# Kernel optimization log

Measured on AMD Instinct MI355X. Metric: run time of the kernel, lower is better.

## Reference

```python
import jax, jax.numpy as jnp
import numpy as np

BOARD = 361  # 19x19 Go board
SEQ = 24     # 8 history boards + 16 move boards


def setup_inputs() -> dict:
    key = jax.random.key(0)
    ks = jax.random.split(key, 12)
    B, H, L = 4096, 256, 2
    s = 1.0 / np.sqrt(H)  # PyTorch LSTM init scale
    u = lambda k, shape: jax.random.uniform(k, shape, jnp.float32, -s, s)
    return {
        "data": jax.random.randint(ks[0], (B, SEQ), 0, BOARD),
        "h0": jax.random.uniform(ks[1], (L * 2, B, H), jnp.float32),
        "c0": jax.random.uniform(ks[2], (L * 2, B, H), jnp.float32),
        "W_ih0": u(ks[3], (2, 4 * H, BOARD)),
        "W_hh0": u(ks[4], (2, 4 * H, H)),
        "b_ih0": u(ks[5], (2, 4 * H)),
        "b_hh0": u(ks[6], (2, 4 * H)),
        "W_ih1": u(ks[7], (2, 4 * H, 2 * H)),
        "W_hh1": u(ks[8], (2, 4 * H, H)),
        "b_ih1": u(ks[9], (2, 4 * H)),
        "b_hh1": u(ks[10], (2, 4 * H)),
    }


def _cell(x, h, c, Wih, Whh, bih, bhh):
    # PyTorch gate order: i, f, g, o
    g = x @ Wih.T + bih + h @ Whh.T + bhh
    i, f, gg, o = jnp.split(g, 4, axis=-1)
    c2 = jax.nn.sigmoid(f) * c + jax.nn.sigmoid(i) * jnp.tanh(gg)
    h2 = jax.nn.sigmoid(o) * jnp.tanh(c2)
    return h2, c2


def reference(data, h0, c0, W_ih0, W_hh0, b_ih0, b_hh0, W_ih1, W_hh1, b_ih1, b_hh1):
    # Fused one-hot construction: pos == -1 -> zero board (replaces nested scatter loops)
    onehot = jnp.where(
        data[..., None] >= 0,
        jax.nn.one_hot(jnp.maximum(data, 0), BOARD, dtype=jnp.float32),
        0.0,
    )  # [B, 24, 361]
    xs = jnp.swapaxes(onehot, 0, 1)  # [24, B, 361]
    layers = [(W_ih0, W_hh0, b_ih0, b_hh0), (W_ih1, W_hh1, b_ih1, b_hh1)]

    def step(carry, x):
        h, c = carry  # [L*2, B, H] each, index = layer*2 + direction
        new_h, new_c = [], []
        inp = x
        for l, (Wih, Whh, bih, bhh) in enumerate(layers):
            hs = []
            for d in range(2):
                idx = l * 2 + d
                h2, c2 = _cell(inp, h[idx], c[idx], Wih[d], Whh[d], bih[d], bhh[d])
                new_h.append(h2)
                new_c.append(c2)
                hs.append(h2)
            inp = jnp.concatenate(hs, axis=-1)  # [B, 2H] fed to next layer
        return (jnp.stack(new_h), jnp.stack(new_c)), inp

    _, ys = jax.lax.scan(step, (h0, c0), xs)  # ys: [24, B, 2H]
    return jnp.swapaxes(ys, 0, 1)  # [B, 24, 2H]
```

## Files before the change

kernel.cpp:

```cpp
#include <hip/hip_runtime.h>


typedef _Float16 f16x8 __attribute__((ext_vector_type(8)));
typedef float f32x4 __attribute__((ext_vector_type(4)));

#define NB 4096
#define SEQ 24
#define HB ((size_t)NB * 256)

__device__ __forceinline__ float bf2f(unsigned short u) {
  return __uint_as_float(((unsigned)u) << 16);
}
__device__ __forceinline__ unsigned short f2bf(float f) {
  unsigned x = __float_as_uint(f);
  x += 0x7fffu + ((x >> 16) & 1u);
  return (unsigned short)(x >> 16);
}
__device__ __forceinline__ float ldw(const void* p, size_t i, int isf32) {
  return isf32 ? ((const float*)p)[i] : bf2f(((const unsigned short*)p)[i]);
}
__device__ __forceinline__ float fsig(float x) {
  return __builtin_amdgcn_rcpf(1.f + __expf(-x));
}
__device__ __forceinline__ float ftanh(float x) {
  float ax = __builtin_fabsf(x);
  float z = __expf(-2.f * ax);
  float r = (1.f - z) * __builtin_amdgcn_rcpf(1.f + z);
  return __builtin_copysignf(r, x);
}
__device__ __forceinline__ void st_h(_Float16* p, float v) {
  unsigned short u = __builtin_bit_cast(unsigned short, (_Float16)v);
  __hip_atomic_store((unsigned short*)p, u, __ATOMIC_RELAXED,
                     __HIP_MEMORY_SCOPE_AGENT);
}

__global__ void k_sniff(const unsigned short* __restrict__ w, int* flag) {
  unsigned short u = w[threadIdx.x * 2];
  int e = (u >> 7) & 0xFF;
  if (e > 123) atomicOr(flag, 1);
}

__global__ void k_prep_wihT0b(const void* __restrict__ Wih0,
                              const void* __restrict__ bih0,
                              const void* __restrict__ bhh0,
                              const int* __restrict__ flag,
                              _Float16* __restrict__ outp) {
  const int isf32 = *flag;
  int idx = blockIdx.x * 256 + threadIdx.x;
  if (idx >= 2 * 362 * 1024) return;
  int n = idx & 1023;
  int p = (idx >> 10) % 362;
  int d = idx / (362 * 1024);
  float v = ldw(bih0, d * 1024 + n, isf32) + ldw(bhh0, d * 1024 + n, isf32);
  if (p < 361) v += ldw(Wih0, (size_t)(d * 1024 + n) * 361 + p, isf32);
  outp[idx] = (_Float16)v;
}

__global__ void k_prep_whh0(const void* __restrict__ Whh0,
                            const int* __restrict__ flag,
                            _Float16* __restrict__ outp) {
  const int isf32 = *flag;
  int idx = blockIdx.x * 256 + threadIdx.x;
  if (idx >= 2 * 1024 * 256) return;
  int jj = idx & 7, lane = (idx >> 3) & 63, kk = (idx >> 9) & 7;
  int nt = (idx >> 12) & 3, g = (idx >> 14) & 3, j = (idx >> 16) & 3, d = (idx >> 18) & 1;
  int row = g * 256 + j * 64 + nt * 16 + (lane & 15);
  int k = kk * 32 + (lane >> 4) * 8 + jj;
  outp[idx] = (_Float16)ldw(Whh0, (size_t)(d * 1024 + row) * 256 + k, isf32);
}

__global__ void k_prep_w1(const void* __restrict__ Wih1,
                          const void* __restrict__ Whh1,
                          const int* __restrict__ flag,
                          _Float16* __restrict__ outp) {
  const int isf32 = *flag;
  int idx = blockIdx.x * 256 + threadIdx.x;
  if (idx >= 2 * 1024 * 768) return;
  int jj = idx & 7, lane = (idx >> 3) & 63, kk = (idx >> 9) & 7;
  int rest = idx >> 12;
  int kc = rest % 3; rest /= 3;
  int nt = rest & 3; rest >>= 2;
  int g = rest & 3; rest >>= 2;
  int j = rest & 3; int d = rest >> 2;
  int row = g * 256 + j * 64 + nt * 16 + (lane & 15);
  int k = kc * 256 + kk * 32 + (lane >> 4) * 8 + jj;
  float v = (k < 512) ? ldw(Wih1, (size_t)(d * 1024 + row) * 512 + k, isf32)
                      : ldw(Whh1, (size_t)(d * 1024 + row) * 256 + (k - 512), isf32);
  outp[idx] = (_Float16)v;
}

__global__ void k_prep_bias1(const void* __restrict__ bih1,
                             const void* __restrict__ bhh1,
                             const int* __restrict__ flag,
                             float* __restrict__ outp) {
  const int isf32 = *flag;
  int idx = blockIdx.x * 256 + threadIdx.x;
  if (idx >= 2048) return;
  outp[idx] = ldw(bih1, idx, isf32) + ldw(bhh1, idx, isf32);
}

__global__ void k_prep_dataT(const int* __restrict__ data, int* __restrict__ dataT) {
  int idx = blockIdx.x * 256 + threadIdx.x;
  if (idx >= NB * SEQ) return;
  int row = idx / SEQ, t = idx % SEQ;
  dataT[t * NB + row] = data[idx];
}

__global__ void k_prep_h(const void* __restrict__ h0, const int* __restrict__ flag,
                         _Float16* __restrict__ h0buf, _Float16* __restrict__ h1buf) {
  const int isf32 = *flag;
  int idx = blockIdx.x * 256 + threadIdx.x;
  if (idx >= 4 * NB * 256) return;
  int ld = idx / (NB * 256);
  int r = idx % (NB * 256);
  _Float16 v = (_Float16)ldw(h0, (size_t)idx, isf32);
  if (ld < 2) h0buf[(size_t)(2 + ld) * HB + r] = v;
  else        h1buf[(size_t)ld * HB + r] = v;
}

__global__ __launch_bounds__(512, 2) void lstm_main(
    const int* __restrict__ dataT,
    const void* __restrict__ c0,
    const _Float16* __restrict__ wihT0b,
    const _Float16* __restrict__ whh0p,
    const _Float16* __restrict__ w1p,
    const float* __restrict__ bias1,
    const int* __restrict__ flag,
    unsigned* bar,
    _Float16* __restrict__ h0buf,
    _Float16* __restrict__ h1buf,
    void* __restrict__ out) {
  const int isf32 = *flag;
  const int tid = threadIdx.x;
  const int lane = tid & 63;
  const int wv = tid >> 6;
  const int n16 = lane & 15;
  const int q = lane >> 4;
  const int bid = blockIdx.x;
  const int rb = bid & 7;
  const int cgi = bid >> 3;
  const int d = cgi >> 4;
  const int hcb = cgi & 15;
  const int hc0 = hcb * 16;
  const int j4 = hcb >> 2, nt4 = hcb & 3;
  const int wrow = rb * 512 + wv * 64;

  extern __shared__ __align__(16) _Float16 lds[];
  _Float16* lw0 = lds;
  _Float16* lw1 = lds + 4 * 4096;
  __shared__ int fast_s;

#pragma unroll
  for (int g = 0; g < 4; ++g) {
    const _Float16* s = whh0p + ((size_t)(((d * 4 + j4) * 4 + g) * 4 + nt4)) * 4096;
    *(f16x8*)&lw0[g * 4096 + tid * 8] = *(const f16x8*)&s[tid * 8];
  }
#pragma unroll
  for (int g = 0; g < 4; ++g)
#pragma unroll
    for (int kc = 0; kc < 3; ++kc) {
      const _Float16* s = w1p + ((size_t)((((d * 4 + j4) * 4 + g) * 4 + nt4) * 3 + kc)) * 4096;
      *(f16x8*)&lw1[(g * 3 + kc) * 4096 + tid * 8] = *(const f16x8*)&s[tid * 8];
    }

  float c0r[4][4], c1r[4][4];
#pragma unroll
  for (int mt = 0; mt < 4; ++mt)
#pragma unroll
    for (int rr = 0; rr < 4; ++rr) {
      int row = wrow + mt * 16 + q * 4 + rr;
      int col = hc0 + n16;
      c0r[mt][rr] = ldw(c0, ((size_t)d * NB + row) * 256 + col, isf32);
      c1r[mt][rr] = ldw(c0, ((size_t)(2 + d) * NB + row) * 256 + col, isf32);
    }
  float bvs[4];
#pragma unroll
  for (int g = 0; g < 4; ++g) bvs[g] = bias1[d * 1024 + g * 256 + hc0 + n16];

  unsigned xcc = __builtin_amdgcn_s_getreg(6164);
  if (tid == 0) {
    unsigned* pre = bar + rb * 32 + 8;
    unsigned* msk = bar + rb * 32 + 16;
    __hip_atomic_fetch_or(msk, 1u << (xcc & 31u), __ATOMIC_RELAXED,
                          __HIP_MEMORY_SCOPE_AGENT);
    asm volatile("s_waitcnt vmcnt(0)" ::: "memory");
    __hip_atomic_fetch_add(pre, 1u, __ATOMIC_RELAXED, __HIP_MEMORY_SCOPE_AGENT);
    while (__hip_atomic_load(pre, __ATOMIC_RELAXED, __HIP_MEMORY_SCOPE_AGENT) < 32u)
      __builtin_amdgcn_s_sleep(1);
    unsigned m = __hip_atomic_load(msk, __ATOMIC_RELAXED, __HIP_MEMORY_SCOPE_AGENT);
    fast_s = ((m & (m - 1u)) == 0u) ? 1 : 0;
  }
  __syncthreads();
  const bool fast = (fast_s != 0);

  for (int p = 0; p <= SEQ; ++p) {
    if (p < SEQ) {
      const _Float16* hsrc = h0buf + ((size_t)(((p & 1) ^ 1) * 2 + d)) * HB;
      f16x8 a[4][8];
#pragma unroll
      for (int mt = 0; mt < 4; ++mt)
#pragma unroll
        for (int kk = 0; kk < 8; ++kk)
          a[mt][kk] = *(const f16x8*)&hsrc[(size_t)(wrow + mt * 16 + n16) * 256 + kk * 32 + q * 8];

      f32x4 acc[4][4];
#pragma unroll
      for (int mt = 0; mt < 4; ++mt) {
        int pos[4];
#pragma unroll
        for (int rr = 0; rr < 4; ++rr) {
          int v = dataT[p * NB + wrow + mt * 16 + q * 4 + rr];
          pos[rr] = (v < 0) ? 361 : v;
        }
#pragma unroll
        for (int g = 0; g < 4; ++g) {
          int col = g * 256 + hc0 + n16;
#pragma unroll
          for (int rr = 0; rr < 4; ++rr)
            acc[mt][g][rr] = (float)wihT0b[((size_t)(d * 362 + pos[rr])) * 1024 + col];
        }
      }
#pragma unroll
      for (int g = 0; g < 4; ++g) {
        f16x8 bf[8];
#pragma unroll
        for (int kk = 0; kk < 8; ++kk)
          bf[kk] = *(const f16x8*)&lw0[g * 4096 + kk * 512 + lane * 8];
#pragma unroll
        for (int mt = 0; mt < 4; ++mt)
#pragma unroll
          for (int kk = 0; kk < 8; ++kk)
            acc[mt][g] = __builtin_amdgcn_mfma_f32_16x16x32_f16(a[mt][kk], bf[kk], acc[mt][g], 0, 0, 0);
      }
      _Float16* hdst = h0buf + ((size_t)((p & 1) * 2 + d)) * HB;
      float hnv[4][4];
#pragma unroll
      for (int mt = 0; mt < 4; ++mt)
#pragma unroll
        for (int rr = 0; rr < 4; ++rr) {
          float iv = fsig(acc[mt][0][rr]);
          float fv = fsig(acc[mt][1][rr]);
          float gv = ftanh(acc[mt][2][rr]);
          float ov = fsig(acc[mt][3][rr]);
          float cn = fv * c0r[mt][rr] + iv * gv;
          c0r[mt][rr] = cn;
          hnv[mt][rr] = ov * ftanh(cn);
        }
      if (fast) {
#pragma unroll
        for (int mt = 0; mt < 4; ++mt)
#pragma unroll
          for (int rr = 0; rr < 4; ++rr)
            hdst[(size_t)(wrow + mt * 16 + q * 4 + rr) * 256 + hc0 + n16] =
                (_Float16)hnv[mt][rr];
      } else {
#pragma unroll
        for (int mt = 0; mt < 4; ++mt)
#pragma unroll
          for (int rr = 0; rr < 4; ++rr)
            st_h(&hdst[(size_t)(wrow + mt * 16 + q * 4 + rr) * 256 + hc0 + n16],
                 hnv[mt][rr]);
      }
    }
    if (p >= 1) {
      const int t = p - 1;
      f32x4 acc[4][4];
#pragma unroll
      for (int mt = 0; mt < 4; ++mt)
#pragma unroll
        for (int g = 0; g < 4; ++g) {
          f32x4 b4 = {bvs[g], bvs[g], bvs[g], bvs[g]};
          acc[mt][g] = b4;
        }
#pragma unroll
      for (int kc = 0; kc < 3; ++kc) {
        const _Float16* base =
            (kc == 0) ? h0buf + ((size_t)((t & 1) * 2 + 0)) * HB
          : (kc == 1) ? h0buf + ((size_t)((t & 1) * 2 + 1)) * HB
                      : h1buf + ((size_t)(((t & 1) ^ 1) * 2 + d)) * HB;
        f16x8 a[4][8];
#pragma unroll
        for (int mt = 0; mt < 4; ++mt)
#pragma unroll
          for (int kk = 0; kk < 8; ++kk)
            a[mt][kk] = *(const f16x8*)&base[(size_t)(wrow + mt * 16 + n16) * 256 + kk * 32 + q * 8];
#pragma unroll
        for (int g = 0; g < 4; ++g) {
          f16x8 bf[8];
#pragma unroll
          for (int kk = 0; kk < 8; ++kk)
            bf[kk] = *(const f16x8*)&lw1[(g * 3 + kc) * 4096 + kk * 512 + lane * 8];
#pragma unroll
          for (int mt = 0; mt < 4; ++mt)
#pragma unroll
            for (int kk = 0; kk < 8; ++kk)
              acc[mt][g] = __builtin_amdgcn_mfma_f32_16x16x32_f16(a[mt][kk], bf[kk], acc[mt][g], 0, 0, 0);
        }
      }
      _Float16* hdst = h1buf + ((size_t)((t & 1) * 2 + d)) * HB;
      float hnv[4][4];
#pragma unroll
      for (int mt = 0; mt < 4; ++mt)
#pragma unroll
        for (int rr = 0; rr < 4; ++rr) {
          float iv = fsig(acc[mt][0][rr]);
          float fv = fsig(acc[mt][1][rr]);
          float gv = ftanh(acc[mt][2][rr]);
          float ov = fsig(acc[mt][3][rr]);
          float cn = fv * c1r[mt][rr] + iv * gv;
          c1r[mt][rr] = cn;
          float hn = ov * ftanh(cn);
          hnv[mt][rr] = hn;
          int row = wrow + mt * 16 + q * 4 + rr;
          size_t oi = ((size_t)row * SEQ + t) * 512 + d * 256 + hc0 + n16;
          if (isf32) __builtin_nontemporal_store(hn, &((float*)out)[oi]);
          else       __builtin_nontemporal_store(f2bf(hn), &((unsigned short*)out)[oi]);
        }
      if (fast) {
#pragma unroll
        for (int mt = 0; mt < 4; ++mt)
#pragma unroll
          for (int rr = 0; rr < 4; ++rr)
            hdst[(size_t)(wrow + mt * 16 + q * 4 + rr) * 256 + hc0 + n16] =
                (_Float16)hnv[mt][rr];
      } else {
#pragma unroll
        for (int mt = 0; mt < 4; ++mt)
#pragma unroll
          for (int rr = 0; rr < 4; ++rr)
            st_h(&hdst[(size_t)(wrow + mt * 16 + q * 4 + rr) * 256 + hc0 + n16],
                 hnv[mt][rr]);
      }
    }
    if (p < SEQ) {
      __syncthreads();
      if (tid == 0) {
        unsigned* ctr = bar + rb * 32;
        __hip_atomic_fetch_add(ctr, 1u, __ATOMIC_RELAXED, __HIP_MEMORY_SCOPE_AGENT);
        const unsigned tgt = 32u * (unsigned)(p + 1);
        while (__hip_atomic_load(ctr, __ATOMIC_RELAXED, __HIP_MEMORY_SCOPE_AGENT) < tgt) {
          __builtin_amdgcn_s_sleep(1);
        }
      }
      __syncthreads();
      if (!fast) __builtin_amdgcn_fence(__ATOMIC_ACQUIRE, "agent");
    }
  }
}

extern "C" void kernel_launch(void* const* d_in, const int* in_sizes, int n_in,
                              void* d_out, int out_size, void* d_ws, size_t ws_size,
                              hipStream_t stream) {
  const int* data = (const int*)d_in[0];
  const void* h0 = d_in[1];
  const void* c0 = d_in[2];
  const void* Wih0 = d_in[3];
  const void* Whh0 = d_in[4];
  const void* bih0 = d_in[5];
  const void* bhh0 = d_in[6];
  const void* Wih1 = d_in[7];
  const void* Whh1 = d_in[8];
  const void* bih1 = d_in[9];
  const void* bhh1 = d_in[10];

  char* ws = (char*)d_ws;
  _Float16* wihT0b = (_Float16*)ws;
  _Float16* whh0p = (_Float16*)(ws + 1482752);
  _Float16* w1p   = (_Float16*)(ws + 2531328);
  float* b1       = (float*)(ws + 5677056);
  int* flag       = (int*)(ws + 5685248);
  unsigned* bar   = (unsigned*)(ws + 5685504);
  int* dataT      = (int*)(ws + 5687552);
  _Float16* h0buf = (_Float16*)(ws + 6080768);
  _Float16* h1buf = (_Float16*)(ws + 14469376);

  hipMemsetAsync(flag, 0, 256 + 2048, stream);
  k_sniff<<<1, 256, 0, stream>>>((const unsigned short*)Wih0, flag);
  k_prep_wihT0b<<<(2 * 362 * 1024 + 255) / 256, 256, 0, stream>>>(Wih0, bih0, bhh0, flag, wihT0b);
  k_prep_whh0<<<(2 * 1024 * 256 + 255) / 256, 256, 0, stream>>>(Whh0, flag, whh0p);
  k_prep_w1<<<(2 * 1024 * 768 + 255) / 256, 256, 0, stream>>>(Wih1, Whh1, flag, w1p);
  k_prep_bias1<<<8, 256, 0, stream>>>(bih1, bhh1, flag, b1);
  k_prep_dataT<<<(NB * SEQ + 255) / 256, 256, 0, stream>>>(data, dataT);
  k_prep_h<<<(4 * NB * 256 + 255) / 256, 256, 0, stream>>>(h0, flag, h0buf, h1buf);

  (void)hipFuncSetAttribute((const void*)lstm_main,
                            hipFuncAttributeMaxDynamicSharedMemorySize, 131072);

  const int* a0 = dataT;
  const void* a1 = c0;
  const _Float16* a2 = wihT0b;
  const _Float16* a3 = whh0p;
  const _Float16* a4 = w1p;
  const float* a5 = b1;
  const int* a6 = flag;
  unsigned* a7 = bar;
  _Float16* a8 = h0buf;
  _Float16* a9 = h1buf;
  void* a10 = d_out;
  void* kargs[] = {&a0, &a1, &a2, &a3, &a4, &a5, &a6, &a7, &a8, &a9, &a10};
  hipLaunchCooperativeKernel((const void*)lstm_main, dim3(256), dim3(512),
                             kargs, 131072, stream);
}
```

Before: 1.678 ms.

## Precompute layer-0 input projection gather into dense buffer before recurrent kernel

Adds a prep kernel that gathers the one-hot-selected rows of the transposed input weights (with biases) for every timestep, batch row and direction into a dense fp16 buffer. The recurrent kernel then initialises accumulators from this buffer with nontemporal loads, replacing the per-step dataT lookup and scattered gather. This takes the dependent index loads off the serial recurrent path, but it costs a 400MB write plus read, and it only runs when the workspace is large enough.

```diff
diff --git a/kernel.cpp b/kernel.cpp
--- a/kernel.cpp
+++ b/kernel.cpp
@@ -32,6 +32,10 @@
   unsigned short u = __builtin_bit_cast(unsigned short, (_Float16)v);
   __hip_atomic_store((unsigned short*)p, u, __ATOMIC_RELAXED,
                      __HIP_MEMORY_SCOPE_AGENT);
+}
+__device__ __forceinline__ float ld_nt_f16(const _Float16* p) {
+  unsigned short u = __builtin_nontemporal_load((const unsigned short*)p);
+  return (float)__builtin_bit_cast(_Float16, u);
 }
 
 __global__ void k_sniff(const unsigned short* __restrict__ w, int* flag) {
@@ -54,6 +58,21 @@
   float v = ldw(bih0, d * 1024 + n, isf32) + ldw(bhh0, d * 1024 + n, isf32);
   if (p < 361) v += ldw(Wih0, (size_t)(d * 1024 + n) * 361 + p, isf32);
   outp[idx] = (_Float16)v;
+}
+
+__global__ void k_prep_xw(const int* __restrict__ data,
+                          const _Float16* __restrict__ wihT0b,
+                          _Float16* __restrict__ xw) {
+  size_t idx = (size_t)blockIdx.x * 256 + threadIdx.x;
+  if (idx >= (size_t)SEQ * NB * 2 * 128) return;
+  int c8 = (int)(idx & 127);
+  int d = (int)((idx >> 7) & 1);
+  int row = (int)((idx >> 8) & (NB - 1));
+  int t = (int)(idx >> 20);
+  int pos = data[row * SEQ + t];
+  if (pos < 0) pos = 361;
+  f16x8 v = *(const f16x8*)&wihT0b[((size_t)(d * 362 + pos)) * 1024 + c8 * 8];
+  __builtin_nontemporal_store(v, (f16x8*)&xw[idx * 8]);
 }
 
 __global__ void k_prep_whh0(const void* __restrict__ Whh0,
@@ -118,8 +137,10 @@
   else        h1buf[(size_t)ld * HB + r] = v;
 }
 
+template <int UXW>
 __global__ __launch_bounds__(512, 2) void lstm_main(
     const int* __restrict__ dataT,
+    const _Float16* __restrict__ xw,
     const void* __restrict__ c0,
     const _Float16* __restrict__ wihT0b,
     const _Float16* __restrict__ whh0p,
@@ -204,20 +225,33 @@
           a[mt][kk] = *(const f16x8*)&hsrc[(size_t)(wrow + mt * 16 + n16) * 256 + kk * 32 + q * 8];
 
       f32x4 acc[4][4];
-#pragma unroll
-      for (int mt = 0; mt < 4; ++mt) {
-        int pos[4];
-#pragma unroll
-        for (int rr = 0; rr < 4; ++rr) {
-          int v = dataT[p * NB + wrow + mt * 16 + q * 4 + rr];
-          pos[rr] = (v < 0) ? 361 : v;
-        }
-#pragma unroll
-        for (int g = 0; g < 4; ++g) {
-          int col = g * 256 + hc0 + n16;
-#pragma unroll
-          for (int rr = 0; rr < 4; ++rr)
-            acc[mt][g][rr] = (float)wihT0b[((size_t)(d * 362 + pos[rr])) * 1024 + col];
+      if constexpr (UXW) {
+#pragma unroll
+        for (int mt = 0; mt < 4; ++mt)
+#pragma unroll
+          for (int g = 0; g < 4; ++g)
+#pragma unroll
+            for (int rr = 0; rr < 4; ++rr) {
+              int row = wrow + mt * 16 + q * 4 + rr;
+              acc[mt][g][rr] = ld_nt_f16(
+                  &xw[(((size_t)p * NB + row) * 2 + d) * 1024 + g * 256 + hc0 + n16]);
+            }
+      } else {
+#pragma unroll
+        for (int mt = 0; mt < 4; ++mt) {
+          int pos[4];
+#pragma unroll
+          for (int rr = 0; rr < 4; ++rr) {
+            int v = dataT[p * NB + wrow + mt * 16 + q * 4 + rr];
+            pos[rr] = (v < 0) ? 361 : v;
+          }
+#pragma unroll
+          for (int g = 0; g < 4; ++g) {
+            int col = g * 256 + hc0 + n16;
+#pragma unroll
+            for (int rr = 0; rr < 4; ++rr)
+              acc[mt][g][rr] = (float)wihT0b[((size_t)(d * 362 + pos[rr])) * 1024 + col];
+          }
         }
       }
 #pragma unroll
@@ -373,6 +407,9 @@
   int* dataT      = (int*)(ws + 5687552);
   _Float16* h0buf = (_Float16*)(ws + 6080768);
   _Float16* h1buf = (_Float16*)(ws + 14469376);
+  _Float16* xw    = (_Float16*)(ws + 22857984);
+  const size_t WS_NEED_XW = 22857984ULL + 402653184ULL;
+  const int use_xw = (ws_size >= WS_NEED_XW) ? 1 : 0;
 
   hipMemsetAsync(flag, 0, 256 + 2048, stream);
   k_sniff<<<1, 256, 0, stream>>>((const unsigned short*)Wih0, flag);
@@ -382,22 +419,33 @@
   k_prep_bias1<<<8, 256, 0, stream>>>(bih1, bhh1, flag, b1);
   k_prep_dataT<<<(NB * SEQ + 255) / 256, 256, 0, stream>>>(data, dataT);
   k_prep_h<<<(4 * NB * 256 + 255) / 256, 256, 0, stream>>>(h0, flag, h0buf, h1buf);
-
-  (void)hipFuncSetAttribute((const void*)lstm_main,
-                            hipFuncAttributeMaxDynamicSharedMemorySize, 131072);
+  if (use_xw) {
+    k_prep_xw<<<98304, 256, 0, stream>>>(data, wihT0b, xw);
+  }
 
   const int* a0 = dataT;
-  const void* a1 = c0;
-  const _Float16* a2 = wihT0b;
-  const _Float16* a3 = whh0p;
-  const _Float16* a4 = w1p;
-  const float* a5 = b1;
-  const int* a6 = flag;
-  unsigned* a7 = bar;
-  _Float16* a8 = h0buf;
-  _Float16* a9 = h1buf;
-  void* a10 = d_out;
-  void* kargs[] = {&a0, &a1, &a2, &a3, &a4, &a5, &a6, &a7, &a8, &a9, &a10};
-  hipLaunchCooperativeKernel((const void*)lstm_main, dim3(256), dim3(512),
-                             kargs, 131072, stream);
-}
+  const _Float16* a1 = xw;
+  const void* a2 = c0;
+  const _Float16* a3 = wihT0b;
+  const _Float16* a4 = whh0p;
+  const _Float16* a5 = w1p;
+  const float* a6 = b1;
+  const int* a7 = flag;
+  unsigned* a8 = bar;
+  _Float16* a9 = h0buf;
+  _Float16* a10 = h1buf;
+  void* a11 = d_out;
+  void* kargs[] = {&a0, &a1, &a2, &a3, &a4, &a5, &a6, &a7, &a8, &a9, &a10, &a11};
+
+  if (use_xw) {
+    (void)hipFuncSetAttribute((const void*)lstm_main<1>,
+                              hipFuncAttributeMaxDynamicSharedMemorySize, 131072);
+    hipLaunchCooperativeKernel((const void*)lstm_main<1>, dim3(256), dim3(512),
+                               kargs, 131072, stream);
+  } else {
+    (void)hipFuncSetAttribute((const void*)lstm_main<0>,
+                              hipFuncAttributeMaxDynamicSharedMemorySize, 131072);
+    hipLaunchCooperativeKernel((const void*)lstm_main<0>, dim3(256), dim3(512),
+                               kargs, 131072, stream);
+  }
+}
```

After: 1.871 ms. 1.12x slower.
